# Kernel optimization log

Hardware: AMD Instinct MI355X
Metric: run time of the kernel (lower is better)

## Reference

```python
import jax, jax.numpy as jnp
import numpy as np


def gcn_conv(x, src, dst, W, b, n_nodes):
    """PyG-style GCNConv: add self-loops, symmetric deg^-1/2 normalization,
    linear transform, scatter-add aggregation to dst, then bias."""
    loop = jnp.arange(n_nodes, dtype=src.dtype)
    s = jnp.concatenate([src, loop])
    d = jnp.concatenate([dst, loop])
    deg = jax.ops.segment_sum(jnp.ones_like(d, x.dtype), d, num_segments=n_nodes)
    dinv = jax.lax.rsqrt(deg)  # deg >= 1 due to self-loops
    norm = dinv[s] * dinv[d]  # [E+N]
    h = x @ W.T  # [N, out]
    msg = h[s] * norm[:, None]  # [E+N, out]
    return jax.ops.segment_sum(msg, d, num_segments=n_nodes) + b


def setup_inputs() -> dict:
    key = jax.random.key(0)
    k = jax.random.split(key, 6)
    N, E, IN, HID, OUT = 100000, 1600000, 128, 128, 64
    x = jax.random.normal(k[0], (N, IN), dtype=jnp.float32)
    edge_index = jax.random.randint(k[1], (2, E), 0, N, dtype=jnp.int64)
    W1 = jax.random.normal(k[2], (HID, IN), dtype=jnp.float32) * 0.05
    b1 = jnp.zeros((HID,), dtype=jnp.float32)
    W2 = jax.random.normal(k[3], (OUT, HID), dtype=jnp.float32) * 0.05
    b2 = jnp.zeros((OUT,), dtype=jnp.float32)
    return {"x": x, "W1": W1, "b1": b1, "W2": W2, "b2": b2, "edge_index": edge_index}


def reference(x, W1, b1, W2, b2, edge_index):
    n_nodes = x.shape[0]
    src, dst = edge_index[0], edge_index[1]
    h = jax.nn.relu(gcn_conv(x, src, dst, W1, b1, n_nodes))
    return gcn_conv(h, src, dst, W2, b2, n_nodes)
```

## Files before the change

kernel.cpp:

```cpp
#include <hip/hip_runtime.h>
#include <hip/hip_bf16.h>


#define IN_F  128
#define HID_F 128
#define OUT_F 64

#define NPB     128
#define MAXBKT  1024
#define CHUNK   2048
#define CAP     4096
#define SLAB    4096

typedef __bf16 bf16_t;
typedef __bf16 bf16x4 __attribute__((ext_vector_type(4)));
typedef __bf16 bf16x8 __attribute__((ext_vector_type(8)));
typedef float  f32x2  __attribute__((ext_vector_type(2)));
typedef float  f32x4  __attribute__((ext_vector_type(4)));
typedef unsigned u32x2 __attribute__((ext_vector_type(2)));
typedef unsigned u32x4 __attribute__((ext_vector_type(4)));

__global__ __launch_bounds__(256) void k_hist(const int* __restrict__ dst, int E,
                                              int* __restrict__ chunkhist, int NBKT,
                                              int pchunks,
                                              const float* __restrict__ W1s,
                                              const float* __restrict__ W2s,
                                              bf16_t* __restrict__ Wdst,
                                              int n1, int n2,
                                              int* __restrict__ bcur) {
    if ((int)blockIdx.x >= pchunks) {
        int i = (blockIdx.x - pchunks) * 256 + threadIdx.x;
        if (i < n1) Wdst[i] = (bf16_t)W1s[i];
        else if (i < n1 + n2) Wdst[i] = (bf16_t)W2s[i - n1];
        else if (i < n1 + n2 + NBKT) bcur[i - n1 - n2] = (i - n1 - n2) * SLAB;
        return;
    }
    __shared__ int cnt[MAXBKT];
    for (int i = threadIdx.x; i < NBKT; i += 256) cnt[i] = 0;
    __syncthreads();
    int base = blockIdx.x * CHUNK;
    for (int i = threadIdx.x; i < CHUNK; i += 256) {
        int e = base + i;
        if (e < E) atomicAdd(&cnt[dst[e] >> 7], 1);
    }
    __syncthreads();
    int* ch = chunkhist + (size_t)blockIdx.x * MAXBKT;
    for (int i = threadIdx.x; i < NBKT; i += 256) ch[i] = cnt[i];
}

__global__ __launch_bounds__(256) void k_part(const int* __restrict__ src,
                                              const int* __restrict__ dst, int E,
                                              int* __restrict__ bcur,
                                              const int* __restrict__ chunkhist,
                                              unsigned* __restrict__ part, int NBKT) {
    __shared__ int cnt[MAXBKT];
    __shared__ int base[MAXBKT];
    const int* ch = chunkhist + (size_t)blockIdx.x * MAXBKT;
    for (int i = threadIdx.x; i < NBKT; i += 256) {
        int c = ch[i];
        base[i] = c ? atomicAdd(&bcur[i], c) : 0;
        cnt[i] = 0;
    }
    __syncthreads();
    int cbase = blockIdx.x * CHUNK;
    for (int i = threadIdx.x; i < CHUNK; i += 256) {
        int e = cbase + i;
        if (e < E) {
            int d = dst[e];
            int b = d >> 7;
            int lp = atomicAdd(&cnt[b], 1);
            part[base[b] + lp] = (unsigned)src[e] | ((unsigned)(d & 127) << 17);
        }
    }
}

__global__ __launch_bounds__(256) void k_bucket(const unsigned* __restrict__ part,
                                                const int* __restrict__ bcur,
                                                int2* __restrict__ off2,
                                                int* __restrict__ col,
                                                float* __restrict__ dinv, int N) {
    __shared__ int lcnt[NPB];
    __shared__ int lexc[NPB];
    __shared__ int lcur[NPB];
    __shared__ int stage[CAP];
    int b = blockIdx.x;
    int t = threadIdx.x;
    int node0 = b * NPB;
    int nb = min(NPB, N - node0);
    int e0s = b * SLAB;
    int cnt = bcur[b] - e0s;
    if (t < NPB) lcnt[t] = 0;
    __syncthreads();
    for (int i = t; i < cnt; i += 256)
        atomicAdd(&lcnt[part[e0s + i] >> 17], 1);
    __syncthreads();
    if (t < NPB) lexc[t] = (lcnt[t] + 7) & ~7;
    __syncthreads();
    for (int ofs = 1; ofs < NPB; ofs <<= 1) {
        int add = (t >= ofs && t < NPB) ? lexc[t - ofs] : 0;
        __syncthreads();
        if (t < NPB) lexc[t] += add;
        __syncthreads();
    }
    if (t < NPB) {
        int pc = (lcnt[t] + 7) & ~7;
        int ex = lexc[t] - pc;
        lcur[t] = ex;
        if (t < nb) {
            off2[node0 + t] = make_int2(e0s + ex, e0s + ex + pc);
            dinv[node0 + t] = rsqrtf((float)lcnt[t] + 1.0f);
        }
    }
    __syncthreads();
    for (int i = t; i < cnt; i += 256) {
        unsigned p = part[e0s + i];
        int dl = p >> 17;
        int sv = (int)(p & 0x1FFFF);
        int lp = atomicAdd(&lcur[dl], 1);
        if (lp < CAP) stage[lp] = sv;
        else col[e0s + lp] = sv;
    }
    __syncthreads();
    if (t < NPB) {
        int en = lexc[t];
        for (int i = lcur[t]; i < en; i++) {
            if (i < CAP) stage[i] = N; else col[e0s + i] = N;
        }
    }
    __syncthreads();
    int tot = lexc[NPB - 1];
    for (int i = t; i < tot && i < CAP; i += 256) col[e0s + i] = stage[i];
}

template <int NCOL, typename TIN>
__global__ __launch_bounds__(256) void k_gemm_mfma(const TIN* __restrict__ X,
                                                   const bf16_t* __restrict__ W,
                                                   const float* __restrict__ scale,
                                                   bf16_t* __restrict__ H, int N) {
    constexpr int CT = NCOL / 16;
    int wv = threadIdx.x >> 6, lane = threadIdx.x & 63;
    int quad = lane >> 4, l16 = lane & 15;
    int row0 = blockIdx.x * 128 + wv * 32;
    f32x4 acc[2][CT] = {};
#pragma unroll
    for (int ks = 0; ks < 4; ks++) {
        int k0 = ks * 32 + quad * 8;
        bf16x8 a[2];
#pragma unroll
        for (int rt = 0; rt < 2; rt++) {
            int r = row0 + rt * 16 + l16;
            if (r >= N) r = N - 1;
            const TIN* p = X + (size_t)r * 128 + k0;
            if constexpr (sizeof(TIN) == 4) {
                f32x4 x0 = *(const f32x4*)p;
                f32x4 x1 = *(const f32x4*)(p + 4);
                bf16x8 tt;
                tt[0] = (bf16_t)x0[0]; tt[1] = (bf16_t)x0[1];
                tt[2] = (bf16_t)x0[2]; tt[3] = (bf16_t)x0[3];
                tt[4] = (bf16_t)x1[0]; tt[5] = (bf16_t)x1[1];
                tt[6] = (bf16_t)x1[2]; tt[7] = (bf16_t)x1[3];
                a[rt] = tt;
            } else {
                a[rt] = *(const bf16x8*)p;
            }
        }
#pragma unroll
        for (int ct = 0; ct < CT; ct++) {
            bf16x8 bfrag = *(const bf16x8*)(W + (size_t)(ct * 16 + l16) * 128 + k0);
#pragma unroll
            for (int rt = 0; rt < 2; rt++)
                acc[rt][ct] = __builtin_amdgcn_mfma_f32_16x16x32_bf16(a[rt], bfrag, acc[rt][ct], 0, 0, 0);
        }
    }
#pragma unroll
    for (int rt = 0; rt < 2; rt++)
#pragma unroll
        for (int r4 = 0; r4 < 4; r4++) {
            int r = row0 + rt * 16 + quad * 4 + r4;
            if (r < N) {
                float sc = scale[r];
#pragma unroll
                for (int ct = 0; ct < CT; ct++)
                    H[(size_t)r * NCOL + ct * 16 + l16] = (bf16_t)(sc * acc[rt][ct][r4]);
            } else if (r == N) {
#pragma unroll
                for (int ct = 0; ct < CT; ct++)
                    H[(size_t)N * NCOL + ct * 16 + l16] = (bf16_t)0.f;
            }
        }
}

template <int ROWE>
__device__ __forceinline__ void gather8(const bf16_t* __restrict__ hp,
                                        const int* __restrict__ col, int e,
                                        u32x4* w) {
    int4 c0 = *(const int4*)(col + e);
    int4 c1 = *(const int4*)(col + e + 4);
    w[0] = *(const u32x4*)(hp + (unsigned)c0.x * (unsigned)ROWE);
    w[1] = *(const u32x4*)(hp + (unsigned)c0.y * (unsigned)ROWE);
    w[2] = *(const u32x4*)(hp + (unsigned)c0.z * (unsigned)ROWE);
    w[3] = *(const u32x4*)(hp + (unsigned)c0.w * (unsigned)ROWE);
    w[4] = *(const u32x4*)(hp + (unsigned)c1.x * (unsigned)ROWE);
    w[5] = *(const u32x4*)(hp + (unsigned)c1.y * (unsigned)ROWE);
    w[6] = *(const u32x4*)(hp + (unsigned)c1.z * (unsigned)ROWE);
    w[7] = *(const u32x4*)(hp + (unsigned)c1.w * (unsigned)ROWE);
}

__device__ __forceinline__ void accum8(const u32x4* w, f32x2* a2) {
#pragma unroll
    for (int u = 0; u < 8; u++)
#pragma unroll
        for (int k = 0; k < 4; k++) {
            f32x2 v;
            v.x = __uint_as_float(w[u][k] << 16);
            v.y = __uint_as_float(w[u][k] & 0xffff0000u);
            a2[k] += v;
        }
}

template <int ROWE, int LPN, bool RELU, typename TOUT>
__global__ __launch_bounds__(256) void k_agg(const bf16_t* __restrict__ h,
                                             const int2* __restrict__ off2,
                                             const int* __restrict__ col,
                                             const float* __restrict__ dinv,
                                             const float* __restrict__ bias,
                                             TOUT* __restrict__ out, int N) {
    constexpr int NPW = 64 / LPN;
    int lane = threadIdx.x & 63;
    int wv = threadIdx.x >> 6;
    int g = lane / LPN, fl = lane % LPN;
    int node = blockIdx.x * (4 * NPW) + wv * NPW + g;
    if (node >= N) return;
    int f = fl * 8;
    const bf16_t* hp = h + f;
    u32x4 ws = *(const u32x4*)(hp + (unsigned)node * (unsigned)ROWE);
    int2 oe = off2[node];
    float di = dinv[node];
    f32x2 a2[4];
#pragma unroll
    for (int k = 0; k < 4; k++) {
        f32x2 v;
        v.x = __uint_as_float(ws[k] << 16);
        v.y = __uint_as_float(ws[k] & 0xffff0000u);
        a2[k] = v;
    }
    int e = oe.x, e1 = oe.y;
    u32x4 wA[8], wB[8];
    bool pend = false;
    if (e < e1) {
        gather8<ROWE>(hp, col, e, wA); e += 8; pend = true;
    }
    while (e < e1) {
        gather8<ROWE>(hp, col, e, wB); e += 8;
        accum8(wA, a2); pend = false;
        if (e < e1) {
            gather8<ROWE>(hp, col, e, wA); e += 8;
            accum8(wB, a2); pend = true;
        } else {
            accum8(wB, a2);
        }
    }
    if (pend) accum8(wA, a2);

    f32x4 b0 = *(const f32x4*)(bias + f);
    f32x4 b1 = *(const f32x4*)(bias + f + 4);
    float r[8];
#pragma unroll
    for (int j = 0; j < 8; j++) {
        float bv = (j < 4) ? b0[j] : b1[j - 4];
        float val = a2[j >> 1][j & 1] * di + bv;
        if (RELU) val = fmaxf(val, 0.f);
        r[j] = val;
    }
    if constexpr (sizeof(TOUT) == 2) {
        bf16x8 v;
#pragma unroll
        for (int j = 0; j < 8; j++) v[j] = (bf16_t)r[j];
        *(bf16x8*)((bf16_t*)out + (size_t)node * ROWE + f) = v;
    } else {
        f32x4 v0 = {r[0], r[1], r[2], r[3]};
        f32x4 v1 = {r[4], r[5], r[6], r[7]};
        *(f32x4*)((float*)out + (size_t)node * ROWE + f) = v0;
        *(f32x4*)((float*)out + (size_t)node * ROWE + f + 4) = v1;
    }
}

extern "C" void kernel_launch(void* const* d_in, const int* in_sizes, int n_in,
                              void* d_out, int out_size, void* d_ws, size_t ws_size,
                              hipStream_t stream) {
    const float* x  = (const float*)d_in[0];
    const float* W1 = (const float*)d_in[1];
    const float* b1 = (const float*)d_in[2];
    const float* W2 = (const float*)d_in[3];
    const float* b2 = (const float*)d_in[4];
    const int*   ei = (const int*)d_in[5];

    int N = in_sizes[0] / IN_F;
    int E = in_sizes[5] / 2;
    const int* src = ei;
    const int* dst = ei + E;
    int NBKT = (N + NPB - 1) / NPB;
    int pchunks = (E + CHUNK - 1) / CHUNK;

    size_t woff = 0;
    auto alloc = [&](size_t bytes) {
        void* p = (char*)d_ws + woff;
        woff += (bytes + 255) & ~(size_t)255;
        return p;
    };
    int*      bcur  = (int*)alloc((size_t)NBKT * 4);
    int*      chist = (int*)alloc((size_t)pchunks * MAXBKT * 4);
    unsigned* part  = (unsigned*)alloc((size_t)NBKT * SLAB * 4);
    int*      col   = (int*)alloc((size_t)NBKT * SLAB * 4);
    int2*     off2  = (int2*)alloc((size_t)N * 8);
    float*    dinv  = (float*)alloc((size_t)N * 4);
    bf16_t*   Wb    = (bf16_t*)alloc((size_t)(HID_F * IN_F + OUT_F * HID_F) * 2);
    bf16_t*   W1b   = Wb;
    bf16_t*   W2b   = Wb + HID_F * IN_F;
    bf16_t*   h1    = (bf16_t*)alloc((size_t)(N + 1) * HID_F * 2);
    bf16_t*   h1r   = (bf16_t*)alloc((size_t)N * HID_F * 2);
    bf16_t*   h2    = h1;
    float*    outp  = (float*)d_out;

    int n1 = HID_F * IN_F, n2 = OUT_F * HID_F;
    int tailblocks = (n1 + n2 + NBKT + 255) / 256;
    k_hist<<<pchunks + tailblocks, 256, 0, stream>>>(dst, E, chist, NBKT, pchunks,
                                                     W1, W2, Wb, n1, n2, bcur);
    k_part<<<pchunks, 256, 0, stream>>>(src, dst, E, bcur, chist, part, NBKT);
    k_bucket<<<NBKT, 256, 0, stream>>>(part, bcur, off2, col, dinv, N);

    int gemm_blocks = (N + 127) / 128;

    k_gemm_mfma<HID_F, float><<<gemm_blocks, 256, 0, stream>>>(x, W1b, dinv, h1, N);
    k_agg<HID_F, 16, true, bf16_t><<<(N + 15) / 16, 256, 0, stream>>>(h1, off2, col, dinv, b1, h1r, N);

    k_gemm_mfma<OUT_F, bf16_t><<<gemm_blocks, 256, 0, stream>>>(h1r, W2b, dinv, h2, N);
    k_agg<OUT_F, 8, false, float><<<(N + 31) / 32, 256, 0, stream>>>(h2, off2, col, dinv, b2, outp, N);
}
```

Measured before the change: 283.9 us.

## Fuse layer-1 aggregation with layer-2 GEMM and stagger bucket atomics

Merges the first aggregation (with bias and ReLU) and the second linear transform into one kernel. Each block aggregates 16 nodes into shared memory and then runs an MFMA 16x64x128 product, so the intermediate h1r never goes to global memory and one launch is dropped. Also simplifies the double-buffered gather loop in k_agg to a single-buffer loop, which gives up some memory-level parallelism. In k_part, each block starts its bucket atomics at a different offset to reduce contention on bcur.

```diff
diff --git a/kernel.cpp b/kernel.cpp
--- a/kernel.cpp
+++ b/kernel.cpp
@@ -56,7 +56,9 @@
     __shared__ int cnt[MAXBKT];
     __shared__ int base[MAXBKT];
     const int* ch = chunkhist + (size_t)blockIdx.x * MAXBKT;
-    for (int i = threadIdx.x; i < NBKT; i += 256) {
+    int off = (int)((blockIdx.x * 331u) % (unsigned)NBKT);
+    for (int j = threadIdx.x; j < NBKT; j += 256) {
+        int i = j + off; if (i >= NBKT) i -= NBKT;
         int c = ch[i];
         base[i] = c ? atomicAdd(&bcur[i], c) : 0;
         cnt[i] = 0;
@@ -216,6 +218,76 @@
             v.y = __uint_as_float(w[u][k] & 0xffff0000u);
             a2[k] += v;
         }
+}
+
+__global__ __launch_bounds__(256) void k_agg_gemm(const bf16_t* __restrict__ h,
+                                                  const int2* __restrict__ off2,
+                                                  const int* __restrict__ col,
+                                                  const float* __restrict__ dinv,
+                                                  const float* __restrict__ bias,
+                                                  const bf16_t* __restrict__ W2,
+                                                  bf16_t* __restrict__ h2, int N) {
+    __shared__ float hl[16][132];
+    __shared__ float dl[16];
+    int lane = threadIdx.x & 63;
+    int wv = threadIdx.x >> 6;
+    int g = lane >> 4, fl = lane & 15;
+    int node0 = blockIdx.x * 16;
+    int node = node0 + wv * 4 + g;
+    bool alive = node < N;
+    int f = fl * 8;
+    const bf16_t* hp = h + f;
+    f32x2 a2[4] = {};
+    float di = 0.f;
+    if (alive) {
+        u32x4 ws = *(const u32x4*)(hp + (unsigned)node * 128u);
+        int2 oe = off2[node];
+        di = dinv[node];
+#pragma unroll
+        for (int k = 0; k < 4; k++) {
+            f32x2 v;
+            v.x = __uint_as_float(ws[k] << 16);
+            v.y = __uint_as_float(ws[k] & 0xffff0000u);
+            a2[k] = v;
+        }
+        u32x4 w[8];
+        for (int e = oe.x; e < oe.y; e += 8) {
+            gather8<128>(hp, col, e, w);
+            accum8(w, a2);
+        }
+    }
+    f32x4 b0 = *(const f32x4*)(bias + f);
+    f32x4 b1 = *(const f32x4*)(bias + f + 4);
+    int lr = wv * 4 + g;
+#pragma unroll
+    for (int j = 0; j < 8; j++) {
+        float bv = (j < 4) ? b0[j] : b1[j - 4];
+        float val = a2[j >> 1][j & 1] * di + bv;
+        hl[lr][f + j] = fmaxf(val, 0.f);
+    }
+    if (fl == 0) dl[lr] = di;
+    __syncthreads();
+
+    int quad = lane >> 4, l16 = lane & 15;
+    f32x4 c4 = {0.f, 0.f, 0.f, 0.f};
+#pragma unroll
+    for (int ks = 0; ks < 4; ks++) {
+        int k0 = ks * 32 + quad * 8;
+        bf16x8 afr;
+#pragma unroll
+        for (int j = 0; j < 8; j++) afr[j] = (bf16_t)hl[l16][k0 + j];
+        bf16x8 bfr = *(const bf16x8*)(W2 + (size_t)(wv * 16 + l16) * 128 + k0);
+        c4 = __builtin_amdgcn_mfma_f32_16x16x32_bf16(afr, bfr, c4, 0, 0, 0);
+    }
+#pragma unroll
+    for (int r4 = 0; r4 < 4; r4++) {
+        int rr = quad * 4 + r4;
+        int gn = node0 + rr;
+        if (gn < N)
+            h2[(size_t)gn * 64 + wv * 16 + l16] = (bf16_t)(dl[rr] * c4[r4]);
+    }
+    if (blockIdx.x == 0 && threadIdx.x < 32)
+        ((unsigned*)h2)[(size_t)N * 32 + threadIdx.x] = 0u;
 }
 
 template <int ROWE, int LPN, bool RELU, typename TOUT>
@@ -244,24 +316,11 @@
         v.y = __uint_as_float(ws[k] & 0xffff0000u);
         a2[k] = v;
     }
-    int e = oe.x, e1 = oe.y;
-    u32x4 wA[8], wB[8];
-    bool pend = false;
-    if (e < e1) {
-        gather8<ROWE>(hp, col, e, wA); e += 8; pend = true;
-    }
-    while (e < e1) {
-        gather8<ROWE>(hp, col, e, wB); e += 8;
-        accum8(wA, a2); pend = false;
-        if (e < e1) {
-            gather8<ROWE>(hp, col, e, wA); e += 8;
-            accum8(wB, a2); pend = true;
-        } else {
-            accum8(wB, a2);
-        }
-    }
-    if (pend) accum8(wA, a2);
-
+    u32x4 w[8];
+    for (int e = oe.x; e < oe.y; e += 8) {
+        gather8<ROWE>(hp, col, e, w);
+        accum8(w, a2);
+    }
     f32x4 b0 = *(const f32x4*)(bias + f);
     f32x4 b1 = *(const f32x4*)(bias + f + 4);
     float r[8];
@@ -318,8 +377,7 @@
     bf16_t*   W1b   = Wb;
     bf16_t*   W2b   = Wb + HID_F * IN_F;
     bf16_t*   h1    = (bf16_t*)alloc((size_t)(N + 1) * HID_F * 2);
-    bf16_t*   h1r   = (bf16_t*)alloc((size_t)N * HID_F * 2);
-    bf16_t*   h2    = h1;
+    bf16_t*   h2b   = (bf16_t*)alloc((size_t)(N + 1) * OUT_F * 2);
     float*    outp  = (float*)d_out;
 
     int n1 = HID_F * IN_F, n2 = OUT_F * HID_F;
@@ -332,8 +390,6 @@
     int gemm_blocks = (N + 127) / 128;
 
     k_gemm_mfma<HID_F, float><<<gemm_blocks, 256, 0, stream>>>(x, W1b, dinv, h1, N);
-    k_agg<HID_F, 16, true, bf16_t><<<(N + 15) / 16, 256, 0, stream>>>(h1, off2, col, dinv, b1, h1r, N);
-
-    k_gemm_mfma<OUT_F, bf16_t><<<gemm_blocks, 256, 0, stream>>>(h1r, W2b, dinv, h2, N);
-    k_agg<OUT_F, 8, false, float><<<(N + 31) / 32, 256, 0, stream>>>(h2, off2, col, dinv, b2, outp, N);
-}
+    k_agg_gemm<<<(N + 15) / 16, 256, 0, stream>>>(h1, off2, col, dinv, b1, W2b, h2b, N);
+    k_agg<OUT_F, 8, false, float><<<(N + 31) / 32, 256, 0, stream>>>(h2b, off2, col, dinv, b2, outp, N);
+}
```

New measurement: 268.3 us. 1.06x faster.

## Store hidden features in 16-column slices so aggregation gathers stay cache-resident

Applied to the files above, without the earlier changes.

Changes the GEMM outputs and the aggregation inputs to a feature-sliced layout of 16 bf16 columns per slice, so each gather touches a 32-byte row in a smaller working set. The aggregation grid is remapped so consecutive blocks cover different slices of the same node chunk. The gather loop drops its software double-buffering in favour of a simple loop, and col loads and output stores use nontemporal hints. The bucket cursors are padded to 16 ints each, and the per-block start offset for the atomics is rotated, to cut atomic contention and false sharing. The cost is more gather requests per edge (one per slice), since each request now moves only 32 bytes, and the aggregation kernel is more complex.

```diff
diff --git a/kernel.cpp b/kernel.cpp
--- a/kernel.cpp
+++ b/kernel.cpp
@@ -32,7 +32,7 @@
         int i = (blockIdx.x - pchunks) * 256 + threadIdx.x;
         if (i < n1) Wdst[i] = (bf16_t)W1s[i];
         else if (i < n1 + n2) Wdst[i] = (bf16_t)W2s[i - n1];
-        else if (i < n1 + n2 + NBKT) bcur[i - n1 - n2] = (i - n1 - n2) * SLAB;
+        else if (i < n1 + n2 + NBKT) bcur[(i - n1 - n2) * 16] = (i - n1 - n2) * SLAB;
         return;
     }
     __shared__ int cnt[MAXBKT];
@@ -56,9 +56,11 @@
     __shared__ int cnt[MAXBKT];
     __shared__ int base[MAXBKT];
     const int* ch = chunkhist + (size_t)blockIdx.x * MAXBKT;
-    for (int i = threadIdx.x; i < NBKT; i += 256) {
+    int off = (int)((blockIdx.x * 331u) % (unsigned)NBKT);
+    for (int j = threadIdx.x; j < NBKT; j += 256) {
+        int i = j + off; if (i >= NBKT) i -= NBKT;
         int c = ch[i];
-        base[i] = c ? atomicAdd(&bcur[i], c) : 0;
+        base[i] = c ? atomicAdd(&bcur[i * 16], c) : 0;
         cnt[i] = 0;
     }
     __syncthreads();
@@ -88,7 +90,7 @@
     int node0 = b * NPB;
     int nb = min(NPB, N - node0);
     int e0s = b * SLAB;
-    int cnt = bcur[b] - e0s;
+    int cnt = bcur[b * 16] - e0s;
     if (t < NPB) lcnt[t] = 0;
     __syncthreads();
     for (int i = t; i < cnt; i += 256)
@@ -132,12 +134,13 @@
     for (int i = t; i < tot && i < CAP; i += 256) col[e0s + i] = stage[i];
 }
 
-template <int NCOL, typename TIN>
+template <int NCOL, typename TIN, bool IN_SLICED>
 __global__ __launch_bounds__(256) void k_gemm_mfma(const TIN* __restrict__ X,
                                                    const bf16_t* __restrict__ W,
                                                    const float* __restrict__ scale,
                                                    bf16_t* __restrict__ H, int N) {
     constexpr int CT = NCOL / 16;
+    size_t sstride = (size_t)(N + 1) * 16;
     int wv = threadIdx.x >> 6, lane = threadIdx.x & 63;
     int quad = lane >> 4, l16 = lane & 15;
     int row0 = blockIdx.x * 128 + wv * 32;
@@ -150,8 +153,12 @@
         for (int rt = 0; rt < 2; rt++) {
             int r = row0 + rt * 16 + l16;
             if (r >= N) r = N - 1;
-            const TIN* p = X + (size_t)r * 128 + k0;
-            if constexpr (sizeof(TIN) == 4) {
+            if constexpr (IN_SLICED) {
+                const bf16_t* p = (const bf16_t*)X + (size_t)(k0 >> 4) * sstride
+                                  + (size_t)r * 16 + (k0 & 15);
+                a[rt] = *(const bf16x8*)p;
+            } else if constexpr (sizeof(TIN) == 4) {
+                const TIN* p = X + (size_t)r * 128 + k0;
                 f32x4 x0 = *(const f32x4*)p;
                 f32x4 x1 = *(const f32x4*)(p + 4);
                 bf16x8 tt;
@@ -161,7 +168,7 @@
                 tt[6] = (bf16_t)x1[2]; tt[7] = (bf16_t)x1[3];
                 a[rt] = tt;
             } else {
-                a[rt] = *(const bf16x8*)p;
+                a[rt] = *(const bf16x8*)(X + (size_t)r * 128 + k0);
             }
         }
 #pragma unroll
@@ -181,11 +188,11 @@
                 float sc = scale[r];
 #pragma unroll
                 for (int ct = 0; ct < CT; ct++)
-                    H[(size_t)r * NCOL + ct * 16 + l16] = (bf16_t)(sc * acc[rt][ct][r4]);
+                    H[(size_t)ct * sstride + (size_t)r * 16 + l16] = (bf16_t)(sc * acc[rt][ct][r4]);
             } else if (r == N) {
 #pragma unroll
                 for (int ct = 0; ct < CT; ct++)
-                    H[(size_t)N * NCOL + ct * 16 + l16] = (bf16_t)0.f;
+                    H[(size_t)ct * sstride + (size_t)N * 16 + l16] = (bf16_t)0.f;
             }
         }
 }
@@ -194,16 +201,16 @@
 __device__ __forceinline__ void gather8(const bf16_t* __restrict__ hp,
                                         const int* __restrict__ col, int e,
                                         u32x4* w) {
-    int4 c0 = *(const int4*)(col + e);
-    int4 c1 = *(const int4*)(col + e + 4);
-    w[0] = *(const u32x4*)(hp + (unsigned)c0.x * (unsigned)ROWE);
-    w[1] = *(const u32x4*)(hp + (unsigned)c0.y * (unsigned)ROWE);
-    w[2] = *(const u32x4*)(hp + (unsigned)c0.z * (unsigned)ROWE);
-    w[3] = *(const u32x4*)(hp + (unsigned)c0.w * (unsigned)ROWE);
-    w[4] = *(const u32x4*)(hp + (unsigned)c1.x * (unsigned)ROWE);
-    w[5] = *(const u32x4*)(hp + (unsigned)c1.y * (unsigned)ROWE);
-    w[6] = *(const u32x4*)(hp + (unsigned)c1.z * (unsigned)ROWE);
-    w[7] = *(const u32x4*)(hp + (unsigned)c1.w * (unsigned)ROWE);
+    u32x4 c0 = __builtin_nontemporal_load((const u32x4*)(col + e));
+    u32x4 c1 = __builtin_nontemporal_load((const u32x4*)(col + e + 4));
+    w[0] = *(const u32x4*)(hp + (size_t)c0[0] * (unsigned)ROWE);
+    w[1] = *(const u32x4*)(hp + (size_t)c0[1] * (unsigned)ROWE);
+    w[2] = *(const u32x4*)(hp + (size_t)c0[2] * (unsigned)ROWE);
+    w[3] = *(const u32x4*)(hp + (size_t)c0[3] * (unsigned)ROWE);
+    w[4] = *(const u32x4*)(hp + (size_t)c1[0] * (unsigned)ROWE);
+    w[5] = *(const u32x4*)(hp + (size_t)c1[1] * (unsigned)ROWE);
+    w[6] = *(const u32x4*)(hp + (size_t)c1[2] * (unsigned)ROWE);
+    w[7] = *(const u32x4*)(hp + (size_t)c1[3] * (unsigned)ROWE);
 }
 
 __device__ __forceinline__ void accum8(const u32x4* w, f32x2* a2) {
@@ -218,22 +225,28 @@
         }
 }
 
-template <int ROWE, int LPN, bool RELU, typename TOUT>
-__global__ __launch_bounds__(256) void k_agg(const bf16_t* __restrict__ h,
-                                             const int2* __restrict__ off2,
-                                             const int* __restrict__ col,
-                                             const float* __restrict__ dinv,
-                                             const float* __restrict__ bias,
-                                             TOUT* __restrict__ out, int N) {
-    constexpr int NPW = 64 / LPN;
+template <int NSL, bool RELU, bool OUT_SLICED, typename TOUT>
+__global__ __launch_bounds__(256) void k_agg_s(const bf16_t* __restrict__ h,
+                                               const int2* __restrict__ off2,
+                                               const int* __restrict__ col,
+                                               const float* __restrict__ dinv,
+                                               const float* __restrict__ bias,
+                                               TOUT* __restrict__ out, int N) {
+    constexpr int LANES8 = 8 / NSL;
+    size_t sstride = (size_t)(N + 1) * 16;
+    int r8 = blockIdx.x & 7;
+    int slice = r8 / LANES8;
+    int sub = r8 % LANES8;
+    int chunk = blockIdx.x >> 3;
+    int node0 = (chunk * LANES8 + sub) * 128;
     int lane = threadIdx.x & 63;
     int wv = threadIdx.x >> 6;
-    int g = lane / LPN, fl = lane % LPN;
-    int node = blockIdx.x * (4 * NPW) + wv * NPW + g;
+    int g = lane >> 1, fl = lane & 1;
+    int node = node0 + wv * 32 + g;
     if (node >= N) return;
     int f = fl * 8;
-    const bf16_t* hp = h + f;
-    u32x4 ws = *(const u32x4*)(hp + (unsigned)node * (unsigned)ROWE);
+    const bf16_t* hp = h + (size_t)slice * sstride + f;
+    u32x4 ws = *(const u32x4*)(hp + (size_t)node * 16u);
     int2 oe = off2[node];
     float di = dinv[node];
     f32x2 a2[4];
@@ -244,26 +257,14 @@
         v.y = __uint_as_float(ws[k] & 0xffff0000u);
         a2[k] = v;
     }
-    int e = oe.x, e1 = oe.y;
-    u32x4 wA[8], wB[8];
-    bool pend = false;
-    if (e < e1) {
-        gather8<ROWE>(hp, col, e, wA); e += 8; pend = true;
-    }
-    while (e < e1) {
-        gather8<ROWE>(hp, col, e, wB); e += 8;
-        accum8(wA, a2); pend = false;
-        if (e < e1) {
-            gather8<ROWE>(hp, col, e, wA); e += 8;
-            accum8(wB, a2); pend = true;
-        } else {
-            accum8(wB, a2);
-        }
-    }
-    if (pend) accum8(wA, a2);
-
-    f32x4 b0 = *(const f32x4*)(bias + f);
-    f32x4 b1 = *(const f32x4*)(bias + f + 4);
+    u32x4 w[8];
+    for (int e = oe.x; e < oe.y; e += 8) {
+        gather8<16>(hp, col, e, w);
+        accum8(w, a2);
+    }
+    const float* bp = bias + slice * 16 + f;
+    f32x4 b0 = *(const f32x4*)bp;
+    f32x4 b1 = *(const f32x4*)(bp + 4);
     float r[8];
 #pragma unroll
     for (int j = 0; j < 8; j++) {
@@ -276,12 +277,13 @@
         bf16x8 v;
 #pragma unroll
         for (int j = 0; j < 8; j++) v[j] = (bf16_t)r[j];
-        *(bf16x8*)((bf16_t*)out + (size_t)node * ROWE + f) = v;
+        __builtin_nontemporal_store(v, (bf16x8*)((bf16_t*)out + (size_t)slice * sstride + (size_t)node * 16 + f));
     } else {
         f32x4 v0 = {r[0], r[1], r[2], r[3]};
         f32x4 v1 = {r[4], r[5], r[6], r[7]};
-        *(f32x4*)((float*)out + (size_t)node * ROWE + f) = v0;
-        *(f32x4*)((float*)out + (size_t)node * ROWE + f + 4) = v1;
+        float* po = (float*)out + (size_t)node * (NSL * 16) + slice * 16 + f;
+        __builtin_nontemporal_store(v0, (f32x4*)po);
+        __builtin_nontemporal_store(v1, (f32x4*)(po + 4));
     }
 }
 
@@ -308,7 +310,7 @@
         woff += (bytes + 255) & ~(size_t)255;
         return p;
     };
-    int*      bcur  = (int*)alloc((size_t)NBKT * 4);
+    int*      bcur  = (int*)alloc((size_t)NBKT * 16 * 4);
     int*      chist = (int*)alloc((size_t)pchunks * MAXBKT * 4);
     unsigned* part  = (unsigned*)alloc((size_t)NBKT * SLAB * 4);
     int*      col   = (int*)alloc((size_t)NBKT * SLAB * 4);
@@ -318,8 +320,8 @@
     bf16_t*   W1b   = Wb;
     bf16_t*   W2b   = Wb + HID_F * IN_F;
     bf16_t*   h1    = (bf16_t*)alloc((size_t)(N + 1) * HID_F * 2);
-    bf16_t*   h1r   = (bf16_t*)alloc((size_t)N * HID_F * 2);
-    bf16_t*   h2    = h1;
+    bf16_t*   h1r   = (bf16_t*)alloc((size_t)(N + 1) * HID_F * 2);
+    bf16_t*   h2b   = (bf16_t*)alloc((size_t)(N + 1) * OUT_F * 2);
     float*    outp  = (float*)d_out;
 
     int n1 = HID_F * IN_F, n2 = OUT_F * HID_F;
@@ -329,11 +331,11 @@
     k_part<<<pchunks, 256, 0, stream>>>(src, dst, E, bcur, chist, part, NBKT);
     k_bucket<<<NBKT, 256, 0, stream>>>(part, bcur, off2, col, dinv, N);
 
-    int gemm_blocks = (N + 127) / 128;
-
-    k_gemm_mfma<HID_F, float><<<gemm_blocks, 256, 0, stream>>>(x, W1b, dinv, h1, N);
-    k_agg<HID_F, 16, true, bf16_t><<<(N + 15) / 16, 256, 0, stream>>>(h1, off2, col, dinv, b1, h1r, N);
-
-    k_gemm_mfma<OUT_F, bf16_t><<<gemm_blocks, 256, 0, stream>>>(h1r, W2b, dinv, h2, N);
-    k_agg<OUT_F, 8, false, float><<<(N + 31) / 32, 256, 0, stream>>>(h2, off2, col, dinv, b2, outp, N);
-}
+    int CH = (N + 127) / 128;
+    int gemm_blocks = CH;
+
+    k_gemm_mfma<HID_F, float, false><<<gemm_blocks, 256, 0, stream>>>(x, W1b, dinv, h1, N);
+    k_agg_s<8, true, true, bf16_t><<<CH * 8, 256, 0, stream>>>(h1, off2, col, dinv, b1, h1r, N);
+    k_gemm_mfma<OUT_F, bf16_t, true><<<gemm_blocks, 256, 0, stream>>>(h1r, W2b, dinv, h2b, N);
+    k_agg_s<4, false, false, float><<<((CH + 1) / 2) * 8, 256, 0, stream>>>(h2b, off2, col, dinv, b2, outp, N);
+}
```

Result: slower. 376.5 us (+32.6%).
